# Kernel optimization log

Hardware: AMD Instinct MI355X
Metric: run time of the kernel (lower is better)

The kernel has to match this reference:

```python
import jax, jax.numpy as jnp
import numpy as np

EPS = 1e-5

def _bn(y, gamma, beta):
    # BatchNorm1d in training mode over the flattened (B*N, C) batch dim.
    m = jnp.mean(y, axis=0)
    v = jnp.var(y, axis=0)  # biased variance, matches torch normalization
    return gamma * (y - m) * jax.lax.rsqrt(v + EPS) + beta

def _hardswish(x):
    return x * jnp.clip(x + 3.0, 0.0, 6.0) / 6.0

def setup_inputs() -> dict:
    key = jax.random.key(0)
    ks = jax.random.split(key, 8)
    B, N, C, H = 16, 784, 384, 8
    res = int(N ** 0.5)  # 28
    inner = 3 * C
    x = jax.random.normal(ks[0], (B, N, C), dtype=jnp.float32)
    Wqkv = jax.random.normal(ks[1], (inner, C), dtype=jnp.float32) * (C ** -0.5)
    g1 = jnp.ones((inner,), jnp.float32) + 0.1 * jax.random.normal(ks[2], (inner,))
    b1 = 0.1 * jax.random.normal(ks[3], (inner,))
    Wproj = jax.random.normal(ks[4], (C, C), dtype=jnp.float32) * (C ** -0.5)
    g2 = jnp.ones((C,), jnp.float32) + 0.1 * jax.random.normal(ks[5], (C,))
    b2 = 0.1 * jax.random.normal(ks[6], (C,))
    biases = 0.02 * jax.random.normal(ks[7], (H, res * res), dtype=jnp.float32)
    # idx[i,j] = |dx|*res + |dy| reproduces torch's encounter-order offset ids
    coords = np.stack(np.meshgrid(np.arange(res), np.arange(res), indexing='ij'), -1).reshape(N, 2)
    d = np.abs(coords[:, None, :] - coords[None, :, :])
    bias_idxs = jnp.asarray(d[..., 0] * res + d[..., 1], dtype=jnp.int32)  # [N,N]
    return {"x": x, "Wqkv": Wqkv, "g1": g1, "b1": b1, "Wproj": Wproj,
            "g2": g2, "b2": b2, "biases": biases, "bias_idxs": bias_idxs}

def reference(x, Wqkv, g1, b1, Wproj, g2, b2, biases, bias_idxs):
    B, N, C = x.shape
    H = biases.shape[0]
    hd = C // H
    scale = hd ** -0.5
    # qkv = LinearNorm(dim, 3*dim)
    y = _bn(x.reshape(B * N, C) @ Wqkv.T, g1, b1)              # [B*N, 3C]
    qkv = y.reshape(B, N, 3, H, hd).transpose(2, 0, 3, 1, 4)   # [3,B,H,N,hd]
    q, k, v = qkv[0], qkv[1], qkv[2]
    attn = jnp.einsum('bhnd,bhmd->bhnm', q, k) * scale         # [B,H,N,N]
    attn = attn + biases[:, bias_idxs][None]                   # gathered rel-pos bias
    attn = jax.nn.softmax(attn, axis=-1)
    o = jnp.einsum('bhnm,bhmd->bhnd', attn, v)                 # [B,H,N,hd]
    o = o.transpose(0, 2, 1, 3).reshape(B, N, C)
    # proj = Hardswish -> LinearNorm(dim, dim)
    o = _hardswish(o).reshape(B * N, C)
    o = _bn(o @ Wproj.T, g2, b2)
    return o.reshape(B, N, C)
```

## Files before the change

### kernel.cpp

```cpp
#include <hip/hip_runtime.h>

#define R_TOTAL 12544
#define NTOK    784
#define CDIM    384
#define INNER   1152
#define NHEAD   8
#define HDIM    48
#define BATCH   16
#define SCALE   0.14433756729740643f
#define LOG2E   1.4426950408889634f
#define SCLOG2E 0.20823509f

typedef unsigned short u16;
typedef unsigned int   u32;
typedef __attribute__((ext_vector_type(8))) short short8;
typedef __attribute__((ext_vector_type(4))) float floatx4;

union V8 { uint4 u; short8 s; u16 h[8]; };

#define OB_OFF     28901376ull
#define ST_OFF     38535168ull

__device__ __forceinline__ float b2f(u16 u) {
    union { float f; u32 i; } v; v.i = ((u32)u) << 16; return v.f;
}
__device__ __forceinline__ u16 f2b(float f) {
    union { float f; u32 i; } v; v.f = f;
    u32 r = v.i + 0x7FFFu + ((v.i >> 16) & 1u);
    return (u16)(r >> 16);
}
__device__ __forceinline__ u32 pk2(float lo, float hi) {
    union { float f; u32 i; } a, b; a.f = lo; b.f = hi;
    u32 ra = a.i + 0x7FFFu + ((a.i >> 16) & 1u);
    u32 rb = b.i + 0x7FFFu + ((b.i >> 16) & 1u);
    return __builtin_amdgcn_perm(rb, ra, 0x07060302u);
}
__device__ __forceinline__ float hswish_f(float v) {
    return v * fminf(fmaxf(v + 3.f, 0.f), 6.f) * (1.f / 6.f);
}

__global__ __launch_bounds__(256) void zero_k(float* __restrict__ p, int n) {
    int i = blockIdx.x * 256 + threadIdx.x;
    if (i < n) p[i] = 0.f;
}

template<int ABF16, int HSW, int OBF16>
__global__ __launch_bounds__(256) void gemm_mfma_k(
    const void* __restrict__ Ap, const float* __restrict__ Bfp,
    void* __restrict__ Cp, float* __restrict__ sums, int M, int Nout, int K)
{
    __shared__ u16 As[128 * 40];
    __shared__ u16 Bs[128 * 40];
    const int t = threadIdx.x;
    const int lane = t & 63, wv = t >> 6;
    const int l15 = lane & 15, quad = lane >> 4;
    const int wm = (wv & 1) * 64, wn = (wv >> 1) * 64;
    const int m0 = blockIdx.y * 128, n0 = blockIdx.x * 128;
    const floatx4 zf = {0.f, 0.f, 0.f, 0.f};

    floatx4 acc[4][4];
    #pragma unroll
    for (int i = 0; i < 4; i++)
        #pragma unroll
        for (int j = 0; j < 4; j++) acc[i][j] = zf;

    for (int k0 = 0; k0 < K; k0 += 32) {
        __syncthreads();
        #pragma unroll
        for (int it = 0; it < 2; it++) {
            const int flat = t + it * 256;
            const int rr = flat >> 2, ss = (flat & 3) * 8;
            uint4 aw;
            if (ABF16) {
                uint4 u = *(const uint4*)((const u16*)Ap + (size_t)(m0 + rr) * K + k0 + ss);
                if (HSW) {
                    aw.x = pk2(hswish_f(b2f((u16)(u.x & 0xffff))), hswish_f(b2f((u16)(u.x >> 16))));
                    aw.y = pk2(hswish_f(b2f((u16)(u.y & 0xffff))), hswish_f(b2f((u16)(u.y >> 16))));
                    aw.z = pk2(hswish_f(b2f((u16)(u.z & 0xffff))), hswish_f(b2f((u16)(u.z >> 16))));
                    aw.w = pk2(hswish_f(b2f((u16)(u.w & 0xffff))), hswish_f(b2f((u16)(u.w >> 16))));
                } else {
                    aw = u;
                }
            } else {
                const float* p = (const float*)Ap + (size_t)(m0 + rr) * K + k0 + ss;
                float4 f0 = *(const float4*)p, f1 = *(const float4*)(p + 4);
                aw.x = pk2(f0.x, f0.y); aw.y = pk2(f0.z, f0.w);
                aw.z = pk2(f1.x, f1.y); aw.w = pk2(f1.z, f1.w);
            }
            *(uint4*)&As[rr * 40 + ss] = aw;
            const float* q = Bfp + (size_t)(n0 + rr) * K + k0 + ss;
            float4 g0 = *(const float4*)q, g1 = *(const float4*)(q + 4);
            uint4 bw;
            bw.x = pk2(g0.x, g0.y); bw.y = pk2(g0.z, g0.w);
            bw.z = pk2(g1.x, g1.y); bw.w = pk2(g1.z, g1.w);
            *(uint4*)&Bs[rr * 40 + ss] = bw;
        }
        __syncthreads();
        short8 af[4], bfr[4];
        #pragma unroll
        for (int mi = 0; mi < 4; mi++)
            af[mi] = *(const short8*)&As[(wm + mi * 16 + l15) * 40 + quad * 8];
        #pragma unroll
        for (int ni = 0; ni < 4; ni++)
            bfr[ni] = *(const short8*)&Bs[(wn + ni * 16 + l15) * 40 + quad * 8];
        #pragma unroll
        for (int mi = 0; mi < 4; mi++)
            #pragma unroll
            for (int ni = 0; ni < 4; ni++)
                acc[mi][ni] = __builtin_amdgcn_mfma_f32_16x16x32_bf16(af[mi], bfr[ni], acc[mi][ni], 0, 0, 0);
    }

    float cs[4] = {0.f, 0.f, 0.f, 0.f}, cq[4] = {0.f, 0.f, 0.f, 0.f};
    #pragma unroll
    for (int mi = 0; mi < 4; mi++) {
        const int mbase = m0 + wm + mi * 16 + quad * 4;
        #pragma unroll
        for (int ni = 0; ni < 4; ni++) {
            const int n = n0 + wn + ni * 16 + l15;
            #pragma unroll
            for (int reg = 0; reg < 4; reg++) {
                size_t off = (size_t)(mbase + reg) * Nout + n;
                float v = acc[mi][ni][reg];
                float vv;
                if (OBF16) {
                    u16 hv = f2b(v);
                    ((u16*)Cp)[off] = hv;
                    vv = b2f(hv);
                } else {
                    ((float*)Cp)[off] = v;
                    vv = v;
                }
                cs[ni] += vv;
                cq[ni] += vv * vv;
            }
        }
    }
    #pragma unroll
    for (int ni = 0; ni < 4; ni++) {
        float s = cs[ni], sq = cq[ni];
        s  += __shfl_xor(s, 16);  s  += __shfl_xor(s, 32);
        sq += __shfl_xor(sq, 16); sq += __shfl_xor(sq, 32);
        if (quad == 0) {
            int col = n0 + wn + ni * 16 + l15;
            atomicAdd(&sums[col], s);
            atomicAdd(&sums[Nout + col], sq);
        }
    }
}

__global__ __launch_bounds__(256) void finalize_bn_k(
    const float* __restrict__ sums, const float* __restrict__ g,
    const float* __restrict__ bvec, float* __restrict__ ab, int Ncols, float invM,
    int sc0, int sc1, float sfac)
{
    int c = blockIdx.x * 256 + threadIdx.x;
    if (c >= Ncols) return;
    float mean = sums[c] * invM;
    float var  = sums[Ncols + c] * invM - mean * mean;
    float a    = g[c] * rsqrtf(var + 1e-5f);
    float f    = (c >= sc0 && c < sc1) ? sfac : 1.f;
    ab[c] = a * f;
    ab[Ncols + c] = (bvec[c] - mean * a) * f;
}

__global__ __launch_bounds__(256) void bn_apply_k(
    float* __restrict__ Z, const float* __restrict__ ab, int Ncols, int total4)
{
    for (int i4 = blockIdx.x * 256 + threadIdx.x; i4 < total4; i4 += gridDim.x * 256) {
        int col = (i4 * 4) % Ncols;
        float4 z  = *(float4*)(Z + (size_t)i4 * 4);
        float4 a4 = *(const float4*)(ab + col);
        float4 b4 = *(const float4*)(ab + Ncols + col);
        z.x = a4.x * z.x + b4.x; z.y = a4.y * z.y + b4.y;
        z.z = a4.z * z.z + b4.z; z.w = a4.w * z.w + b4.w;
        *(float4*)(Z + (size_t)i4 * 4) = z;
    }
}

__global__ __launch_bounds__(256) void bn_apply_bf16_k(
    u16* __restrict__ Z, const float* __restrict__ ab, int Ncols, int total8)
{
    int i8 = blockIdx.x * 256 + threadIdx.x;
    if (i8 >= total8) return;
    int col = (i8 * 8) % Ncols;
    uint4 u = *(uint4*)(Z + (size_t)i8 * 8);
    float4 A0 = *(const float4*)(ab + col),         A1 = *(const float4*)(ab + col + 4);
    float4 B0 = *(const float4*)(ab + Ncols + col), B1 = *(const float4*)(ab + Ncols + col + 4);
    uint4 o;
    o.x = pk2(fmaf(b2f((u16)(u.x & 0xffff)), A0.x, B0.x), fmaf(b2f((u16)(u.x >> 16)), A0.y, B0.y));
    o.y = pk2(fmaf(b2f((u16)(u.y & 0xffff)), A0.z, B0.z), fmaf(b2f((u16)(u.y >> 16)), A0.w, B0.w));
    o.z = pk2(fmaf(b2f((u16)(u.z & 0xffff)), A1.x, B1.x), fmaf(b2f((u16)(u.z >> 16)), A1.y, B1.y));
    o.w = pk2(fmaf(b2f((u16)(u.w & 0xffff)), A1.z, B1.z), fmaf(b2f((u16)(u.w >> 16)), A1.w, B1.w));
    *(uint4*)(Z + (size_t)i8 * 8) = o;
}

__device__ __forceinline__ uint4 transpose8x8_u16(uint4 v, int g) {
    u32 r0 = v.x, r1 = v.y, r2 = v.z, r3 = v.w;
    {
        u32 t0 = (u32)__shfl_xor((int)r2, 4);
        u32 t1 = (u32)__shfl_xor((int)r3, 4);
        u32 t2 = (u32)__shfl_xor((int)r0, 4);
        u32 t3 = (u32)__shfl_xor((int)r1, 4);
        bool gb2 = (g >> 2) & 1;
        r0 = gb2 ? t0 : r0;
        r1 = gb2 ? t1 : r1;
        r2 = gb2 ? r2 : t2;
        r3 = gb2 ? r3 : t3;
    }
    {
        u32 t0 = (u32)__shfl_xor((int)r1, 2);
        u32 t1 = (u32)__shfl_xor((int)r0, 2);
        u32 t2 = (u32)__shfl_xor((int)r3, 2);
        u32 t3 = (u32)__shfl_xor((int)r2, 2);
        bool gb1 = (g >> 1) & 1;
        r0 = gb1 ? t0 : r0;
        r1 = gb1 ? r1 : t1;
        r2 = gb1 ? t2 : r2;
        r3 = gb1 ? r3 : t3;
    }
    {
        u32 t0 = (u32)__shfl_xor((int)r0, 1);
        u32 t1 = (u32)__shfl_xor((int)r1, 1);
        u32 t2 = (u32)__shfl_xor((int)r2, 1);
        u32 t3 = (u32)__shfl_xor((int)r3, 1);
        if (g & 1) {
            r0 = (r0 & 0xFFFF0000u) | (t0 >> 16);
            r1 = (r1 & 0xFFFF0000u) | (t1 >> 16);
            r2 = (r2 & 0xFFFF0000u) | (t2 >> 16);
            r3 = (r3 & 0xFFFF0000u) | (t3 >> 16);
        } else {
            r0 = (r0 & 0x0000FFFFu) | (t0 << 16);
            r1 = (r1 & 0x0000FFFFu) | (t1 << 16);
            r2 = (r2 & 0x0000FFFFu) | (t2 << 16);
            r3 = (r3 & 0x0000FFFFu) | (t3 << 16);
        }
    }
    return make_uint4(r0, r1, r2, r3);
}

__global__ __launch_bounds__(256) void attn_mfma_k(
    const u16* __restrict__ Y,
    const float* __restrict__ biases, const int* __restrict__ idxs,
    u16* __restrict__ O)
{
    __shared__ u16 vt[2][6 * 64 * 8];
    __shared__ u16 psm[4][2][2 * 64 * 8];
    __shared__ float hb[NTOK];

    const int t = threadIdx.x;
    const int lane = t & 63, wv = t >> 6;
    const int l15 = lane & 15, quad = lane >> 4;
    const int g8 = lane & 7, sg = lane >> 3;
    const int bh = blockIdx.x;
    const int b = bh >> 3, h = bh & 7;
    const int n0 = blockIdx.y * 128;
    const int bN = b * NTOK;
    const int colQ = h * HDIM, colK = CDIM + colQ, colV = 2 * CDIM + colQ;
    const floatx4 zf = {0.f, 0.f, 0.f, 0.f};

    if (t < 196) {
        float4 v = *(const float4*)(biases + (size_t)h * NTOK + (t << 2));
        v.x *= LOG2E; v.y *= LOG2E; v.z *= LOG2E; v.w *= LOG2E;
        *(float4*)&hb[t << 2] = v;
    }

    int qv[2], qr[2];
    #pragma unroll
    for (int qh = 0; qh < 2; qh++) {
        qv[qh] = n0 + qh * 64 + wv * 16 + l15;
        qr[qh] = qv[qh] < NTOK ? qv[qh] : NTOK - 1;
    }
    const int* idxrow[2] = { idxs + (size_t)qr[0] * NTOK, idxs + (size_t)qr[1] * NTOK };

    short8 qf[2][2];
    #pragma unroll
    for (int qh = 0; qh < 2; qh++) {
        V8 a0, a1;
        a1.u = make_uint4(0u, 0u, 0u, 0u);
        const u16* src = Y + (size_t)(bN + qr[qh]) * INNER + colQ;
        a0.u = *(const uint4*)(src + quad * 8);
        if (quad < 2) a1.u = *(const uint4*)(src + 32 + quad * 8);
        qf[qh][0] = a0.s; qf[qh][1] = a1.s;
    }

    const bool ownB = (wv < 2);
    const int dsA = wv, dsB = 4 + wv;
    const int dA = dsA * 8 + g8, dB = dsB * 8 + g8;
    const int vaddrA = (((dA >> 4) * 2 + (sg >> 2)) * 64 + (sg & 3) * 16 + (dA & 15)) * 8;
    const int vaddrB = (((dB >> 4) * 2 + (sg >> 2)) * 64 + (sg & 3) * 16 + (dB & 15)) * 8;

    V8 pvA, pvB;
    {
        const u16* src = Y + (size_t)(bN + lane) * INNER + colV;
        pvA.u = *(const uint4*)(src + dsA * 8);
        if (ownB) pvB.u = *(const uint4*)(src + dsB * 8);
        *(uint4*)&vt[0][vaddrA] = transpose8x8_u16(pvA.u, g8);
        if (ownB) *(uint4*)&vt[0][vaddrB] = transpose8x8_u16(pvB.u, g8);
    }

    V8 kfr[4][2];
    #pragma unroll
    for (int sub = 0; sub < 4; sub++) {
        const u16* src = Y + (size_t)(bN + sub * 16 + l15) * INNER + colK;
        kfr[sub][0].u = *(const uint4*)(src + quad * 8);
        kfr[sub][1].u = *(const uint4*)(src + 32 + quad * 8);
    }

    float lsum[2] = {0.f, 0.f};
    floatx4 oacc[2][3];
    #pragma unroll
    for (int qh = 0; qh < 2; qh++)
        #pragma unroll
        for (int i = 0; i < 3; i++) oacc[qh][i] = zf;

    const int psbase = ((quad >> 1) * 16 + l15) * 8 + (quad & 1) * 4;

    for (int mt = 0; mt < 13; mt++) {
        const int m0k = mt * 64;
        const bool tail = (m0k == 768);
        __syncthreads();

        int4 ivc[2][4];
        #pragma unroll
        for (int qh = 0; qh < 2; qh++)
            #pragma unroll
            for (int sub = 0; sub < 4; sub++) {
                int kb = m0k + sub * 16 + quad * 4;
                kb = kb < NTOK - 4 ? kb : NTOK - 4;
                ivc[qh][sub] = *(const int4*)(idxrow[qh] + kb);
            }

        V8 kn[4][2];
        const bool more = (mt + 1 < 13);
        if (more) {
            const int mn = m0k + 64;
            #pragma unroll
            for (int sub = 0; sub < 4; sub++) {
                int key = mn + sub * 16 + l15;
                int kr  = key < NTOK ? key : NTOK - 1;
                const u16* src = Y + (size_t)(bN + kr) * INNER + colK;
                kn[sub][0].u = *(const uint4*)(src + quad * 8);
                kn[sub][1].u = *(const uint4*)(src + 32 + quad * 8);
            }
            int kv = mn + lane; kv = kv < NTOK ? kv : NTOK - 1;
            const u16* src = Y + (size_t)(bN + kv) * INNER + colV;
            pvA.u = *(const uint4*)(src + dsA * 8);
            if (ownB) pvB.u = *(const uint4*)(src + dsB * 8);
        }

        #pragma unroll
        for (int qh = 0; qh < 2; qh++) {
            floatx4 sf[4];
            #pragma unroll
            for (int sub = 0; sub < 4; sub++) {
                floatx4 c = zf;
                c = __builtin_amdgcn_mfma_f32_16x16x32_bf16(kfr[sub][0].s, qf[qh][0], c, 0, 0, 0);
                c = __builtin_amdgcn_mfma_f32_16x16x32_bf16(kfr[sub][1].s, qf[qh][1], c, 0, 0, 0);
                sf[sub] = c;
            }
            #pragma unroll
            for (int sub = 0; sub < 4; sub++) {
                const int4 iv = ivc[qh][sub];
                float a0 = sf[sub][0] + hb[iv.x];
                float a1 = sf[sub][1] + hb[iv.y];
                float a2 = sf[sub][2] + hb[iv.z];
                float a3 = sf[sub][3] + hb[iv.w];
                float pr[4];
                asm("v_exp_f32 %0, %1" : "=v"(pr[0]) : "v"(a0));
                asm("v_exp_f32 %0, %1" : "=v"(pr[1]) : "v"(a1));
                asm("v_exp_f32 %0, %1" : "=v"(pr[2]) : "v"(a2));
                asm("v_exp_f32 %0, %1" : "=v"(pr[3]) : "v"(a3));
                if (tail) {
                    const int kb0 = m0k + sub * 16 + quad * 4;
                    #pragma unroll
                    for (int reg = 0; reg < 4; reg++)
                        if (kb0 + reg >= NTOK) pr[reg] = 0.f;
                }
                lsum[qh] += (pr[0] + pr[1]) + (pr[2] + pr[3]);
                int addr = psbase + (sub >> 1) * 512 + (sub & 1) * 256;
                *(uint2*)&psm[wv][qh][addr] = make_uint2(pk2(pr[0], pr[1]), pk2(pr[2], pr[3]));
            }
        }

        if (more) {
            u16* vtb = vt[(mt + 1) & 1];
            *(uint4*)&vtb[vaddrA] = transpose8x8_u16(pvA.u, g8);
            if (ownB) *(uint4*)&vtb[vaddrB] = transpose8x8_u16(pvB.u, g8);
        }

        const u16* vtb = vt[mt & 1];
        #pragma unroll
        for (int kc = 0; kc < 2; kc++) {
            short8 pb0 = *(const short8*)&psm[wv][0][(kc * 64 + lane) * 8];
            short8 pb1 = *(const short8*)&psm[wv][1][(kc * 64 + lane) * 8];
            #pragma unroll
            for (int ns = 0; ns < 3; ns++) {
                short8 va = *(const short8*)&vtb[((ns * 2 + kc) * 64 + lane) * 8];
                oacc[0][ns] = __builtin_amdgcn_mfma_f32_16x16x32_bf16(va, pb0, oacc[0][ns], 0, 0, 0);
                oacc[1][ns] = __builtin_amdgcn_mfma_f32_16x16x32_bf16(va, pb1, oacc[1][ns], 0, 0, 0);
            }
        }

        if (more) {
            #pragma unroll
            for (int sub = 0; sub < 4; sub++) {
                kfr[sub][0] = kn[sub][0];
                kfr[sub][1] = kn[sub][1];
            }
        }
    }

    #pragma unroll
    for (int qh = 0; qh < 2; qh++) {
        float ls = lsum[qh];
        ls += __shfl_xor(ls, 16);
        ls += __shfl_xor(ls, 32);
        if (qv[qh] < NTOK) {
            float rl = 1.f / ls;
            u16* dst = O + (size_t)(bN + qv[qh]) * CDIM + colQ;
            #pragma unroll
            for (int ns = 0; ns < 3; ns++)
                #pragma unroll
                for (int reg = 0; reg < 4; reg++)
                    dst[ns * 16 + quad * 4 + reg] = f2b(hswish_f(oacc[qh][ns][reg] * rl));
        }
    }
}

extern "C" void kernel_launch(void* const* d_in, const int* in_sizes, int n_in,
                              void* d_out, int out_size, void* d_ws, size_t ws_size,
                              hipStream_t stream)
{
    const float* x     = (const float*)d_in[0];
    const float* Wqkv  = (const float*)d_in[1];
    const float* g1    = (const float*)d_in[2];
    const float* b1    = (const float*)d_in[3];
    const float* Wproj = (const float*)d_in[4];
    const float* g2    = (const float*)d_in[5];
    const float* b2    = (const float*)d_in[6];
    const float* bias  = (const float*)d_in[7];
    const int*   idxs  = (const int*)d_in[8];
    float* out = (float*)d_out;
    char*  wsb = (char*)d_ws;

    u16*   Yb  = (u16*)wsb;
    u16*   Ob  = (u16*)(wsb + OB_OFF);
    float* S1  = (float*)(wsb + ST_OFF);
    float* AB1 = S1 + 2304;
    float* S2  = AB1 + 2304;
    float* AB2 = S2 + 768;

    zero_k<<<24, 256, 0, stream>>>(S1, 6144);

    gemm_mfma_k<0, 0, 1><<<dim3(INNER / 128, R_TOTAL / 128), 256, 0, stream>>>(
        x, Wqkv, Yb, S1, R_TOTAL, INNER, CDIM);

    finalize_bn_k<<<(INNER + 255) / 256, 256, 0, stream>>>(
        S1, g1, b1, AB1, INNER, 1.f / R_TOTAL, CDIM, 2 * CDIM, SCLOG2E);
    bn_apply_bf16_k<<<(R_TOTAL * INNER / 8 + 255) / 256, 256, 0, stream>>>(
        Yb, AB1, INNER, R_TOTAL * INNER / 8);

    attn_mfma_k<<<dim3(NHEAD * BATCH, 7), 256, 0, stream>>>(Yb, bias, idxs, Ob);

    gemm_mfma_k<1, 0, 0><<<dim3(CDIM / 128, R_TOTAL / 128), 256, 0, stream>>>(
        Ob, Wproj, out, S2, R_TOTAL, CDIM, CDIM);

    finalize_bn_k<<<(CDIM + 255) / 256, 256, 0, stream>>>(
        S2, g2, b2, AB2, CDIM, 1.f / R_TOTAL, 0, 0, 1.f);
    bn_apply_k<<<1024, 256, 0, stream>>>(out, AB2, CDIM, (R_TOTAL * CDIM) / 4);
}
```

Baseline: 251.3 us.

## Store QKV in head-major contiguous layout for attention loads

The QKV GEMM epilogue now writes its bf16 output in a [batch, head, q/k/v, token, 48] layout instead of row-major [token, 1152]. Each head's Q, K and V then sit in a contiguous 75 KB segment, so attention loads read dense 96-byte rows rather than strided slices of 2304-byte rows. The BN-apply kernel recomputes each element's column from the new layout. The cost is scattered epilogue stores in the GEMM (16 lanes write 32 contiguous bytes) and extra index arithmetic in both kernels.

Measured after the change: 242.2 us. 1.04x faster.

```diff
diff --git a/kernel.cpp b/kernel.cpp
--- a/kernel.cpp
+++ b/kernel.cpp
@@ -7,6 +7,7 @@
 #define NHEAD   8
 #define HDIM    48
 #define BATCH   16
+#define HSEG    37632
 #define SCALE   0.14433756729740643f
 #define LOG2E   1.4426950408889634f
 #define SCLOG2E 0.20823509f
@@ -44,7 +45,7 @@
     if (i < n) p[i] = 0.f;
 }
 
-template<int ABF16, int HSW, int OBF16>
+template<int ABF16, int HSW, int OBF16, int HEADM>
 __global__ __launch_bounds__(256) void gemm_mfma_k(
     const void* __restrict__ Ap, const float* __restrict__ Bfp,
     void* __restrict__ Cp, float* __restrict__ sums, int M, int Nout, int K)
@@ -114,20 +115,43 @@
     #pragma unroll
     for (int mi = 0; mi < 4; mi++) {
         const int mbase = m0 + wm + mi * 16 + quad * 4;
+        int bb_[4], nn_[4];
+        if (HEADM) {
+            #pragma unroll
+            for (int reg = 0; reg < 4; reg++) {
+                int m = mbase + reg;
+                int bv = ((m >> 4) * 1338) >> 16;
+                bb_[reg] = bv;
+                nn_[reg] = m - bv * 784;
+            }
+        }
         #pragma unroll
         for (int ni = 0; ni < 4; ni++) {
-            const int n = n0 + wn + ni * 16 + l15;
+            const int c0 = n0 + wn + ni * 16;
+            const int n = c0 + l15;
+            int part = 0, hcol = 0, d0 = 0;
+            if (HEADM) {
+                part = c0 / 384;
+                int rem = c0 - part * 384;
+                hcol = rem / 48;
+                d0 = rem - hcol * 48;
+            }
             #pragma unroll
             for (int reg = 0; reg < 4; reg++) {
-                size_t off = (size_t)(mbase + reg) * Nout + n;
                 float v = acc[mi][ni][reg];
                 float vv;
                 if (OBF16) {
                     u16 hv = f2b(v);
+                    size_t off;
+                    if (HEADM)
+                        off = (size_t)((bb_[reg] * 8 + hcol) * 3 + part) * HSEG
+                            + (size_t)nn_[reg] * 48 + d0 + l15;
+                    else
+                        off = (size_t)(mbase + reg) * Nout + n;
                     ((u16*)Cp)[off] = hv;
                     vv = b2f(hv);
                 } else {
-                    ((float*)Cp)[off] = v;
+                    ((float*)Cp)[(size_t)(mbase + reg) * Nout + n] = v;
                     vv = v;
                 }
                 cs[ni] += vv;
@@ -178,14 +202,20 @@
 }
 
 __global__ __launch_bounds__(256) void bn_apply_bf16_k(
-    u16* __restrict__ Z, const float* __restrict__ ab, int Ncols, int total8)
+    u16* __restrict__ Z, const float* __restrict__ ab, int total8)
 {
     int i8 = blockIdx.x * 256 + threadIdx.x;
     if (i8 >= total8) return;
-    int col = (i8 * 8) % Ncols;
+    int e0  = i8 * 8;
+    int seg = e0 / HSEG;
+    int rem = e0 - seg * HSEG;
+    int d0  = rem % 48;
+    int part = seg % 3;
+    int hh   = (seg / 3) & 7;
+    int col  = part * 384 + hh * 48 + d0;
     uint4 u = *(uint4*)(Z + (size_t)i8 * 8);
-    float4 A0 = *(const float4*)(ab + col),         A1 = *(const float4*)(ab + col + 4);
-    float4 B0 = *(const float4*)(ab + Ncols + col), B1 = *(const float4*)(ab + Ncols + col + 4);
+    float4 A0 = *(const float4*)(ab + col),        A1 = *(const float4*)(ab + col + 4);
+    float4 B0 = *(const float4*)(ab + 1152 + col), B1 = *(const float4*)(ab + 1152 + col + 4);
     uint4 o;
     o.x = pk2(fmaf(b2f((u16)(u.x & 0xffff)), A0.x, B0.x), fmaf(b2f((u16)(u.x >> 16)), A0.y, B0.y));
     o.y = pk2(fmaf(b2f((u16)(u.y & 0xffff)), A0.z, B0.z), fmaf(b2f((u16)(u.y >> 16)), A0.w, B0.w));
@@ -255,8 +285,11 @@
     const int b = bh >> 3, h = bh & 7;
     const int n0 = blockIdx.y * 128;
     const int bN = b * NTOK;
-    const int colQ = h * HDIM, colK = CDIM + colQ, colV = 2 * CDIM + colQ;
     const floatx4 zf = {0.f, 0.f, 0.f, 0.f};
+
+    const u16* Qb = Y + (size_t)(bh * 3) * HSEG;
+    const u16* Kb = Qb + HSEG;
+    const u16* Vb = Qb + 2 * HSEG;
 
     if (t < 196) {
         float4 v = *(const float4*)(biases + (size_t)h * NTOK + (t << 2));
@@ -277,7 +310,7 @@
     for (int qh = 0; qh < 2; qh++) {
         V8 a0, a1;
         a1.u = make_uint4(0u, 0u, 0u, 0u);
-        const u16* src = Y + (size_t)(bN + qr[qh]) * INNER + colQ;
+        const u16* src = Qb + (size_t)qr[qh] * 48;
         a0.u = *(const uint4*)(src + quad * 8);
         if (quad < 2) a1.u = *(const uint4*)(src + 32 + quad * 8);
         qf[qh][0] = a0.s; qf[qh][1] = a1.s;
@@ -291,7 +324,7 @@
 
     V8 pvA, pvB;
     {
-        const u16* src = Y + (size_t)(bN + lane) * INNER + colV;
+        const u16* src = Vb + (size_t)lane * 48;
         pvA.u = *(const uint4*)(src + dsA * 8);
         if (ownB) pvB.u = *(const uint4*)(src + dsB * 8);
         *(uint4*)&vt[0][vaddrA] = transpose8x8_u16(pvA.u, g8);
@@ -301,7 +334,7 @@
     V8 kfr[4][2];
     #pragma unroll
     for (int sub = 0; sub < 4; sub++) {
-        const u16* src = Y + (size_t)(bN + sub * 16 + l15) * INNER + colK;
+        const u16* src = Kb + (size_t)(sub * 16 + l15) * 48;
         kfr[sub][0].u = *(const uint4*)(src + quad * 8);
         kfr[sub][1].u = *(const uint4*)(src + 32 + quad * 8);
     }
@@ -338,12 +371,12 @@
             for (int sub = 0; sub < 4; sub++) {
                 int key = mn + sub * 16 + l15;
                 int kr  = key < NTOK ? key : NTOK - 1;
-                const u16* src = Y + (size_t)(bN + kr) * INNER + colK;
+                const u16* src = Kb + (size_t)kr * 48;
                 kn[sub][0].u = *(const uint4*)(src + quad * 8);
                 kn[sub][1].u = *(const uint4*)(src + 32 + quad * 8);
             }
             int kv = mn + lane; kv = kv < NTOK ? kv : NTOK - 1;
-            const u16* src = Y + (size_t)(bN + kv) * INNER + colV;
+            const u16* src = Vb + (size_t)kv * 48;
             pvA.u = *(const uint4*)(src + dsA * 8);
             if (ownB) pvB.u = *(const uint4*)(src + dsB * 8);
         }
@@ -417,7 +450,7 @@
         ls += __shfl_xor(ls, 32);
         if (qv[qh] < NTOK) {
             float rl = 1.f / ls;
-            u16* dst = O + (size_t)(bN + qv[qh]) * CDIM + colQ;
+            u16* dst = O + (size_t)(bN + qv[qh]) * CDIM + h * HDIM;
             #pragma unroll
             for (int ns = 0; ns < 3; ns++)
                 #pragma unroll
@@ -452,17 +485,17 @@
 
     zero_k<<<24, 256, 0, stream>>>(S1, 6144);
 
-    gemm_mfma_k<0, 0, 1><<<dim3(INNER / 128, R_TOTAL / 128), 256, 0, stream>>>(
+    gemm_mfma_k<0, 0, 1, 1><<<dim3(INNER / 128, R_TOTAL / 128), 256, 0, stream>>>(
         x, Wqkv, Yb, S1, R_TOTAL, INNER, CDIM);
 
     finalize_bn_k<<<(INNER + 255) / 256, 256, 0, stream>>>(
         S1, g1, b1, AB1, INNER, 1.f / R_TOTAL, CDIM, 2 * CDIM, SCLOG2E);
     bn_apply_bf16_k<<<(R_TOTAL * INNER / 8 + 255) / 256, 256, 0, stream>>>(
-        Yb, AB1, INNER, R_TOTAL * INNER / 8);
+        Yb, AB1, R_TOTAL * INNER / 8);
 
     attn_mfma_k<<<dim3(NHEAD * BATCH, 7), 256, 0, stream>>>(Yb, bias, idxs, Ob);
 
-    gemm_mfma_k<1, 0, 0><<<dim3(CDIM / 128, R_TOTAL / 128), 256, 0, stream>>>(
+    gemm_mfma_k<1, 0, 0, 0><<<dim3(CDIM / 128, R_TOTAL / 128), 256, 0, stream>>>(
         Ob, Wproj, out, S2, R_TOTAL, CDIM, CDIM);
 
     finalize_bn_k<<<(CDIM + 255) / 256, 256, 0, stream>>>(
```
